# Kernel tuning notes

Measured on AMD Instinct MI355X. Metric: run time of the kernel, lower is better.

## Reference

```python
import jax, jax.numpy as jnp
import numpy as np

N_NODES = 50000
N_EDGES = 800000
K_HOPS = 4
F_IN, F_HID, A_DIM = 6, 128, 3


def gcn_norm(edge_index, edge_weight, num_nodes):
    # TAGConv(normalize=True) uses gcn_norm WITHOUT added self-loops:
    # norm = D^{-1/2}[src] * w * D^{-1/2}[dst], deg computed at target (col).
    row, col = edge_index[0], edge_index[1]
    deg = jax.ops.segment_sum(edge_weight, col, num_segments=num_nodes)
    deg_inv_sqrt = jnp.where(deg > 0, jax.lax.rsqrt(deg), 0.0)
    return deg_inv_sqrt[row] * edge_weight * deg_inv_sqrt[col]


def tag_conv(x, edge_index, norm_w, W, b):
    # out = sum_{k=0..K} (A_hat^k x) @ W[k] + b ; W: [K+1, in, out]
    row, col = edge_index[0], edge_index[1]
    out = x @ W[0]
    xk = x
    for k in range(1, W.shape[0]):
        # one sparse propagation hop: gather at src, scale, scatter-add at dst
        xk = jax.ops.segment_sum(norm_w[:, None] * xk[row], col, num_segments=x.shape[0])
        out = out + xk @ W[k]
    return out + b


def setup_inputs() -> dict:
    key = jax.random.key(0)
    ks = jax.random.split(key, 5)
    x = jax.random.normal(ks[0], (N_NODES, F_IN), dtype=jnp.float32)
    edge_index = jax.random.randint(ks[1], (2, N_EDGES), 0, N_NODES, dtype=jnp.int32)
    edge_weight = jax.random.uniform(ks[2], (N_EDGES,), dtype=jnp.float32)
    s1 = float(1.0 / np.sqrt(F_IN))
    s2 = float(1.0 / np.sqrt(F_HID))
    W1 = jax.random.uniform(ks[3], (K_HOPS + 1, F_IN, F_HID), minval=-s1, maxval=s1, dtype=jnp.float32)
    b1 = jnp.zeros((F_HID,), jnp.float32)
    W2 = jax.random.uniform(ks[4], (K_HOPS + 1, F_HID, 2 * A_DIM), minval=-s2, maxval=s2, dtype=jnp.float32)
    b2 = jnp.zeros((2 * A_DIM,), jnp.float32)
    return {"x": x, "edge_index": edge_index, "edge_weight": edge_weight,
            "W1": W1, "b1": b1, "W2": W2, "b2": b2}


def reference(x, edge_index, edge_weight, W1, b1, W2, b2):
    norm_w = gcn_norm(edge_index, edge_weight, x.shape[0])
    h = jax.nn.relu(tag_conv(x, edge_index, norm_w, W1, b1))
    out = tag_conv(h, edge_index, norm_w, W2, b2)
    mu = jnp.tanh(out[..., :A_DIM])
    logvar = jnp.tanh(out[..., A_DIM:])
    sigma = jnp.exp(2.0 * logvar)
    return mu, sigma
```

## Files before the change

### kernel.cpp

```cpp
#include <hip/hip_runtime.h>

#define NN 50000
#define NE 800000
#define KH 4
#define FIN 6
#define FH 128
#define FO 6
#define ADIM 3
#define NN6 (NN * 6)
#define NN8 (NN * 8)
#define NBKT 196
#define EPB 2048
#define NPB 391
#define CAP 5120
#define ROWMASK 0xFFFFFu
#define GFUSE 2048
#define NEPAD (NE + NBKT * 256)

typedef unsigned int u32;

struct __align__(8) Edge { u32 r; float w; };

__global__ void bucket_hist(const int* __restrict__ col, u32* __restrict__ ghist) {
    __shared__ u32 h[NBKT];
    for (int t = threadIdx.x; t < NBKT; t += 256) h[t] = 0;
    __syncthreads();
    int base = blockIdx.x * EPB;
#pragma unroll
    for (int i = 0; i < EPB / 256; ++i) {
        int e = base + i * 256 + threadIdx.x;
        if (e < NE) atomicAdd(&h[((u32)col[e]) >> 8], 1u);
    }
    __syncthreads();
    for (int t = threadIdx.x; t < NBKT; t += 256)
        if (h[t]) atomicAdd(&ghist[t], h[t]);
}

__global__ void bucket_scan(const u32* __restrict__ ghist, u32* __restrict__ bbase,
                            u32* __restrict__ bcur) {
    __shared__ u32 sh[256];
    int t = threadIdx.x;
    u32 v = (t < NBKT) ? ghist[t] : 0;
    sh[t] = v;
    __syncthreads();
    for (int off = 1; off < 256; off <<= 1) {
        u32 u = (t >= off) ? sh[t - off] : 0;
        __syncthreads();
        sh[t] += u;
        __syncthreads();
    }
    if (t < NBKT) { bbase[t] = sh[t] - v; bcur[t] = sh[t] - v; }
    if (t == NBKT - 1) bbase[NBKT] = sh[t];
}

__global__ __launch_bounds__(256) void partition_kernel(
        const int* __restrict__ row, const int* __restrict__ col,
        const float* __restrict__ w, u32* __restrict__ bcur,
        Edge* __restrict__ etmp) {
    __shared__ u32 hcnt[NBKT];
    __shared__ u32 hloc[NBKT];
    __shared__ u32 hglb[NBKT];
    __shared__ u32 smeta[EPB];
    __shared__ float swt[EPB];
    __shared__ u32 sgid[EPB];
    __shared__ u32 sc[256];
    for (int t = threadIdx.x; t < NBKT; t += 256) hcnt[t] = 0;
    __syncthreads();
    int base = blockIdx.x * EPB;
    u32 m_[8]; float w_[8]; u32 b_[8]; u32 rk_[8]; int v_[8];
#pragma unroll
    for (int i = 0; i < 8; ++i) {
        int e = base + i * 256 + threadIdx.x;
        v_[i] = e < NE;
        if (v_[i]) {
            u32 c = (u32)col[e];
            u32 r = (u32)row[e];
            b_[i] = c >> 8;
            m_[i] = ((c & 255u) << 20) | r;
            w_[i] = w[e];
            rk_[i] = atomicAdd(&hcnt[b_[i]], 1u);
        }
    }
    __syncthreads();
    {
        int t = threadIdx.x;
        u32 v = (t < NBKT) ? hcnt[t] : 0;
        sc[t] = v;
        __syncthreads();
        for (int off = 1; off < 256; off <<= 1) {
            u32 u = (t >= off) ? sc[t - off] : 0;
            __syncthreads();
            sc[t] += u;
            __syncthreads();
        }
        if (t < NBKT) hloc[t] = sc[t] - v;
    }
    __syncthreads();
    for (int t = threadIdx.x; t < NBKT; t += 256)
        if (hcnt[t]) hglb[t] = atomicAdd(&bcur[t], hcnt[t]);
    __syncthreads();
#pragma unroll
    for (int i = 0; i < 8; ++i) if (v_[i]) {
        u32 slot = hloc[b_[i]] + rk_[i];
        smeta[slot] = m_[i];
        swt[slot] = w_[i];
        sgid[slot] = hglb[b_[i]] + rk_[i];
    }
    __syncthreads();
    int tot = NE - base; if (tot > EPB) tot = EPB;
    for (int s = threadIdx.x; s < tot; s += 256) {
        Edge ed; ed.r = smeta[s]; ed.w = swt[s];
        etmp[sgid[s]] = ed;
    }
}

__global__ __launch_bounds__(256) void bucket_csr(
        const u32* __restrict__ bbase, const Edge* __restrict__ etmp,
        Edge* __restrict__ edges, int* __restrict__ offs, int* __restrict__ eoff,
        float* __restrict__ dinv) {
    int b = blockIdx.x;
    int t = threadIdx.x;
    u32 s = bbase[b], e = bbase[b + 1];
    int cnt = (int)(e - s);
    u32 rb = s + (u32)b * 256u;
    int node0 = b << 8;
    int nloc = NN - node0; if (nloc > 256) nloc = 256;
    __shared__ u32 ncnt[256];
    __shared__ float nsum[256];
    __shared__ u32 ncur[256];
    __shared__ u32 sc[256];
    __shared__ Edge stage[CAP];
    ncnt[t] = 0; nsum[t] = 0.f;
    __syncthreads();
    for (int i = t; i < cnt; i += 256) {
        Edge ed = etmp[s + i];
        u32 cl = ed.r >> 20;
        atomicAdd(&ncnt[cl], 1u);
        atomicAdd(&nsum[cl], ed.w);
    }
    __syncthreads();
    u32 v = ncnt[t];
    u32 pv = (v + 1u) & ~1u;
    sc[t] = pv;
    __syncthreads();
    for (int off = 1; off < 256; off <<= 1) {
        u32 u = (t >= off) ? sc[t - off] : 0;
        __syncthreads();
        sc[t] += u;
        __syncthreads();
    }
    u32 excl = sc[t] - pv;
    u32 ptot = sc[255];
    ncur[t] = excl;
    if (t < nloc) {
        offs[node0 + t] = (int)(rb + excl);
        eoff[node0 + t] = (int)(rb + excl + pv);
        float d = nsum[t];
        dinv[node0 + t] = d > 0.f ? rsqrtf(d) : 0.f;
    }
    __syncthreads();
    for (int i = t; i < cnt; i += 256) {
        Edge ed = etmp[s + i];
        u32 cl = ed.r >> 20;
        u32 slot = atomicAdd(&ncur[cl], 1u);
        Edge ce; ce.r = ed.r & ROWMASK; ce.w = ed.w;
        if (slot < CAP) stage[slot] = ce;
        else edges[rb + slot] = ce;
    }
    if (t < nloc && (v & 1u)) {
        u32 slot = excl + v;
        Edge ce; ce.r = 0u; ce.w = 0.f;
        if (slot < CAP) stage[slot] = ce;
        else edges[rb + slot] = ce;
    }
    __syncthreads();
    int lim = (int)(ptot < CAP ? ptot : CAP);
    for (int i = t; i < lim; i += 256) edges[rb + i] = stage[i];
}

__global__ void pad_x(const float* __restrict__ x, float* __restrict__ xpad) {
    int t = blockIdx.x * blockDim.x + threadIdx.x;
    if (t >= NN8) return;
    int n = t >> 3, c = t & 7;
    xpad[t] = (c < 6) ? x[n * 6 + c] : 0.f;
}

__device__ __forceinline__ void gather6(const float* __restrict__ base, u32 r,
                                        int xst, int xof, float w,
                                        float& a0, float& a1, float& a2,
                                        float& a3, float& a4, float& a5) {
    const float* xr = base + (size_t)r * xst + xof;
    float4 u = *(const float4*)xr;
    float2 v = *(const float2*)(xr + 4);
    a0 += w * u.x; a1 += w * u.y; a2 += w * u.z;
    a3 += w * u.w; a4 += w * v.x; a5 += w * v.y;
}

__global__ void hop8(const int* __restrict__ offs, const int* __restrict__ eoff,
                     const Edge* __restrict__ edges,
                     const float* __restrict__ xprev, int xst, int xof,
                     const float* __restrict__ yadd,
                     float* __restrict__ xnext) {
    int t = blockIdx.x * blockDim.x + threadIdx.x;
    int n = t >> 3, j = t & 7;
    if (n >= NN) return;
    int s = offs[n], e = eoff[n];
    float a0 = 0.f, a1 = 0.f, a2 = 0.f, a3 = 0.f, a4 = 0.f, a5 = 0.f;
    for (int i = s + 2 * j; i < e; i += 16) {
        int4 ep = *(const int4*)&edges[i];
        gather6(xprev, (u32)ep.x, xst, xof, __int_as_float(ep.y), a0, a1, a2, a3, a4, a5);
        gather6(xprev, (u32)ep.z, xst, xof, __int_as_float(ep.w), a0, a1, a2, a3, a4, a5);
    }
#pragma unroll
    for (int d = 1; d < 8; d <<= 1) {
        a0 += __shfl_xor(a0, d); a1 += __shfl_xor(a1, d); a2 += __shfl_xor(a2, d);
        a3 += __shfl_xor(a3, d); a4 += __shfl_xor(a4, d); a5 += __shfl_xor(a5, d);
    }
    if (j < 6) {
        float v = j == 0 ? a0 : j == 1 ? a1 : j == 2 ? a2 : j == 3 ? a3 : j == 4 ? a4 : a5;
        if (yadd) v += yadd[(size_t)n * 32 + j];
        xnext[n * 8 + j] = v;
    }
}

__global__ void hop8_norm(const int* __restrict__ offs, const int* __restrict__ eoff,
                          Edge* __restrict__ edges,
                          const float* __restrict__ dinv, const float* __restrict__ xpad,
                          float* __restrict__ xnext) {
    int t = blockIdx.x * blockDim.x + threadIdx.x;
    int n = t >> 3, j = t & 7;
    if (n >= NN) return;
    int s = offs[n], e = eoff[n];
    float dn = dinv[n];
    float a0 = 0.f, a1 = 0.f, a2 = 0.f, a3 = 0.f, a4 = 0.f, a5 = 0.f;
    for (int i = s + 2 * j; i < e; i += 16) {
        int4 ep = *(const int4*)&edges[i];
        u32 r0 = (u32)ep.x, r1 = (u32)ep.z;
        float wn0 = __int_as_float(ep.y) * dn * dinv[r0];
        float wn1 = __int_as_float(ep.w) * dn * dinv[r1];
        ep.y = __float_as_int(wn0); ep.w = __float_as_int(wn1);
        *(int4*)&edges[i] = ep;
        gather6(xpad, r0, 8, 0, wn0, a0, a1, a2, a3, a4, a5);
        gather6(xpad, r1, 8, 0, wn1, a0, a1, a2, a3, a4, a5);
    }
#pragma unroll
    for (int d = 1; d < 8; d <<= 1) {
        a0 += __shfl_xor(a0, d); a1 += __shfl_xor(a1, d); a2 += __shfl_xor(a2, d);
        a3 += __shfl_xor(a3, d); a4 += __shfl_xor(a4, d); a5 += __shfl_xor(a5, d);
    }
    if (j < 6) {
        float v = j == 0 ? a0 : j == 1 ? a1 : j == 2 ? a2 : j == 3 ? a3 : j == 4 ? a4 : a5;
        xnext[n * 8 + j] = v;
    }
}

__global__ void hop8_final(const int* __restrict__ offs, const int* __restrict__ eoff,
                           const Edge* __restrict__ edges,
                           const float* __restrict__ xprev, const float* __restrict__ y0,
                           float* __restrict__ out) {
    int t = blockIdx.x * blockDim.x + threadIdx.x;
    int n = t >> 3, j = t & 7;
    if (n >= NN) return;
    int s = offs[n], e = eoff[n];
    float a0 = 0.f, a1 = 0.f, a2 = 0.f, a3 = 0.f, a4 = 0.f, a5 = 0.f;
    for (int i = s + 2 * j; i < e; i += 16) {
        int4 ep = *(const int4*)&edges[i];
        gather6(xprev, (u32)ep.x, 8, 0, __int_as_float(ep.y), a0, a1, a2, a3, a4, a5);
        gather6(xprev, (u32)ep.z, 8, 0, __int_as_float(ep.w), a0, a1, a2, a3, a4, a5);
    }
#pragma unroll
    for (int d = 1; d < 8; d <<= 1) {
        a0 += __shfl_xor(a0, d); a1 += __shfl_xor(a1, d); a2 += __shfl_xor(a2, d);
        a3 += __shfl_xor(a3, d); a4 += __shfl_xor(a4, d); a5 += __shfl_xor(a5, d);
    }
    if (j < 6) {
        float v = j == 0 ? a0 : j == 1 ? a1 : j == 2 ? a2 : j == 3 ? a3 : j == 4 ? a4 : a5;
        v += y0[(size_t)n * 32 + j];
        float tv = tanhf(v);
        if (j < ADIM) out[n * ADIM + j] = tv;
        else          out[NN * ADIM + n * ADIM + (j - ADIM)] = expf(2.f * tv);
    }
}

__global__ __launch_bounds__(256) void fused_dense_kernel(
        const float* __restrict__ x, const float* __restrict__ xs,
        const float* __restrict__ W1, const float* __restrict__ b1,
        const float* __restrict__ W2, const float* __restrict__ b2,
        float* __restrict__ ys) {
    __shared__ float sin_[2][32];
    __shared__ float sh[2][128];
    int t = threadIdx.x;
    int f = t & 127, half = t >> 7;
    float w1r[30];
#pragma unroll
    for (int i = 0; i < 30; ++i) w1r[i] = W1[i * FH + f];
    float b1r = b1[f];
    bool bact = t < 240;
    int bn = t / 120;
    int rem = t % 120;
    int ka = rem >> 2;
    int q  = rem & 3;
    int k2 = ka / 6, a2 = ka - k2 * 6;
    float w2r[32];
#pragma unroll
    for (int i = 0; i < 32; ++i)
        w2r[i] = bact ? W2[((size_t)k2 * FH + q * 32 + i) * FO + a2] : 0.f;
    float badd = (bact && k2 == 0 && q == 0) ? b2[a2] : 0.f;

    for (int n0 = blockIdx.x * 2; n0 < NN; n0 += GFUSE * 2) {
        if (t < 60) {
            int nn = t / 30, c = t - nn * 30;
            int n = n0 + nn;
            float v;
            if (c < 6) v = x[n * 6 + c];
            else       v = xs[(size_t)((c - 6) / 6) * NN8 + n * 8 + (c - 6) % 6];
            sin_[nn][c] = v;
        }
        __syncthreads();
        {
            float s = b1r;
#pragma unroll
            for (int i = 0; i < 30; ++i) s += sin_[half][i] * w1r[i];
            sh[half][f] = s > 0.f ? s : 0.f;
        }
        __syncthreads();
        if (bact) {
            float s = badd;
            const float* hr = &sh[bn][q * 32];
#pragma unroll
            for (int i = 0; i < 32; ++i) s += hr[i] * w2r[i];
            s += __shfl_xor(s, 1);
            s += __shfl_xor(s, 2);
            if (q == 0) ys[(size_t)(n0 + bn) * 32 + ka] = s;
        }
    }
}

extern "C" void kernel_launch(void* const* d_in, const int* in_sizes, int n_in,
                              void* d_out, int out_size, void* d_ws, size_t ws_size,
                              hipStream_t stream) {
    const float* x  = (const float*)d_in[0];
    const int*   ei = (const int*)d_in[1];
    const float* ew = (const float*)d_in[2];
    const float* W1 = (const float*)d_in[3];
    const float* b1 = (const float*)d_in[4];
    const float* W2 = (const float*)d_in[5];
    const float* b2 = (const float*)d_in[6];
    float* out = (float*)d_out;

    const int* row = ei;
    const int* col = ei + NE;

    Edge*  etmp  = (Edge*)d_ws;
    Edge*  edges = etmp + NE;
    float* xpad  = (float*)(edges + NEPAD);
    float* xs    = xpad + NN8;
    float* ys    = xs + (size_t)KH * NN8;
    float* za    = ys + (size_t)NN * 32;
    float* zb    = za + NN8;
    u32*   ghist = (u32*)(zb + NN8);
    u32*   bbase = ghist + NBKT;
    u32*   bcur  = bbase + NBKT + 1;
    int*   offs  = (int*)(bcur + NBKT);
    int*   eoff  = offs + NN;
    float* dinv  = (float*)(eoff + NN);

    const int B = 256;
    const int gHop = (NN * 8 + B - 1) / B;
    const int gPad = (NN8 + B - 1) / B;

    hipMemsetAsync(ghist, 0, NBKT * sizeof(u32), stream);
    bucket_hist<<<NPB, B, 0, stream>>>(col, ghist);
    bucket_scan<<<1, B, 0, stream>>>(ghist, bbase, bcur);
    partition_kernel<<<NPB, B, 0, stream>>>(row, col, ew, bcur, etmp);
    bucket_csr<<<NBKT, B, 0, stream>>>(bbase, etmp, edges, offs, eoff, dinv);
    pad_x<<<gPad, B, 0, stream>>>(x, xpad);

    hop8_norm<<<gHop, B, 0, stream>>>(offs, eoff, edges, dinv, xpad, xs);
    for (int k = 2; k <= KH; ++k)
        hop8<<<gHop, B, 0, stream>>>(offs, eoff, edges,
                                     xs + (size_t)(k - 2) * NN8, 8, 0, nullptr,
                                     xs + (size_t)(k - 1) * NN8);

    fused_dense_kernel<<<GFUSE, B, 0, stream>>>(x, xs, W1, b1, W2, b2, ys);

    hop8<<<gHop, B, 0, stream>>>(offs, eoff, edges, ys, 32, 24, ys + 18, za);
    hop8<<<gHop, B, 0, stream>>>(offs, eoff, edges, za, 8, 0, ys + 12, zb);
    hop8<<<gHop, B, 0, stream>>>(offs, eoff, edges, zb, 8, 0, ys + 6, za);
    hop8_final<<<gHop, B, 0, stream>>>(offs, eoff, edges, za, ys, out);
}
```

Before: 166.5 us.

## Pack edges and node features into fp16 and use 4 lanes per node

Edges are packed into a single 32-bit word holding a 16-bit row index and an fp16 weight. Node feature vectors in the propagation hops are stored as 8 halfs (16 bytes) instead of 8 floats. Hop kernels now use 4 lanes per node, each handling 4 edges per int4 load, and the CSR padding is raised to multiples of 4. The aim is to halve gather and edge-stream bandwidth in the memory-bound hops, at the cost of fp16 rounding error accumulating over 8 hops.

```diff
diff --git a/kernel.cpp b/kernel.cpp
--- a/kernel.cpp
+++ b/kernel.cpp
@@ -12,14 +12,26 @@
 #define NBKT 196
 #define EPB 2048
 #define NPB 391
-#define CAP 5120
+#define CAP 6144
 #define ROWMASK 0xFFFFFu
 #define GFUSE 2048
-#define NEPAD (NE + NBKT * 256)
+#define NEPAD (NE + NBKT * 1024)
 
 typedef unsigned int u32;
+typedef _Float16 f16;
+typedef f16 f16x8 __attribute__((ext_vector_type(8)));
 
 struct __align__(8) Edge { u32 r; float w; };
+
+__device__ __forceinline__ float h2f_bits(u32 hb) {
+    union { unsigned short us; f16 h; } c; c.us = (unsigned short)hb; return (float)c.h;
+}
+__device__ __forceinline__ u32 f2h_bits(float f) {
+    union { unsigned short us; f16 h; } c; c.h = (f16)f; return (u32)c.us;
+}
+__device__ __forceinline__ u32 pack2(float a, float b) {
+    return f2h_bits(a) | (f2h_bits(b) << 16);
+}
 
 __global__ void bucket_hist(const int* __restrict__ col, u32* __restrict__ ghist) {
     __shared__ u32 h[NBKT];
@@ -116,20 +128,20 @@
 
 __global__ __launch_bounds__(256) void bucket_csr(
         const u32* __restrict__ bbase, const Edge* __restrict__ etmp,
-        Edge* __restrict__ edges, int* __restrict__ offs, int* __restrict__ eoff,
+        u32* __restrict__ edges, int* __restrict__ offs, int* __restrict__ eoff,
         float* __restrict__ dinv) {
     int b = blockIdx.x;
     int t = threadIdx.x;
     u32 s = bbase[b], e = bbase[b + 1];
     int cnt = (int)(e - s);
-    u32 rb = s + (u32)b * 256u;
+    u32 rb = s + (u32)b * 1024u;
     int node0 = b << 8;
     int nloc = NN - node0; if (nloc > 256) nloc = 256;
     __shared__ u32 ncnt[256];
     __shared__ float nsum[256];
     __shared__ u32 ncur[256];
     __shared__ u32 sc[256];
-    __shared__ Edge stage[CAP];
+    __shared__ u32 stage[CAP];
     ncnt[t] = 0; nsum[t] = 0.f;
     __syncthreads();
     for (int i = t; i < cnt; i += 256) {
@@ -140,7 +152,7 @@
     }
     __syncthreads();
     u32 v = ncnt[t];
-    u32 pv = (v + 1u) & ~1u;
+    u32 pv = (v + 3u) & ~3u;
     sc[t] = pv;
     __syncthreads();
     for (int off = 1; off < 256; off <<= 1) {
@@ -163,130 +175,139 @@
         Edge ed = etmp[s + i];
         u32 cl = ed.r >> 20;
         u32 slot = atomicAdd(&ncur[cl], 1u);
-        Edge ce; ce.r = ed.r & ROWMASK; ce.w = ed.w;
-        if (slot < CAP) stage[slot] = ce;
-        else edges[rb + slot] = ce;
-    }
-    if (t < nloc && (v & 1u)) {
-        u32 slot = excl + v;
-        Edge ce; ce.r = 0u; ce.w = 0.f;
-        if (slot < CAP) stage[slot] = ce;
-        else edges[rb + slot] = ce;
+        u32 pw = (ed.r & ROWMASK) | (f2h_bits(ed.w) << 16);
+        if (slot < CAP) stage[slot] = pw;
+        else edges[rb + slot] = pw;
+    }
+    if (t < nloc) {
+        for (u32 slot = excl + v; slot < excl + pv; ++slot) {
+            if (slot < CAP) stage[slot] = 0u;
+            else edges[rb + slot] = 0u;
+        }
     }
     __syncthreads();
     int lim = (int)(ptot < CAP ? ptot : CAP);
     for (int i = t; i < lim; i += 256) edges[rb + i] = stage[i];
 }
 
-__global__ void pad_x(const float* __restrict__ x, float* __restrict__ xpad) {
+__global__ void pad_x(const float* __restrict__ x, f16* __restrict__ xpad) {
     int t = blockIdx.x * blockDim.x + threadIdx.x;
     if (t >= NN8) return;
     int n = t >> 3, c = t & 7;
-    xpad[t] = (c < 6) ? x[n * 6 + c] : 0.f;
-}
-
-__device__ __forceinline__ void gather6(const float* __restrict__ base, u32 r,
-                                        int xst, int xof, float w,
-                                        float& a0, float& a1, float& a2,
-                                        float& a3, float& a4, float& a5) {
-    const float* xr = base + (size_t)r * xst + xof;
-    float4 u = *(const float4*)xr;
-    float2 v = *(const float2*)(xr + 4);
-    a0 += w * u.x; a1 += w * u.y; a2 += w * u.z;
-    a3 += w * u.w; a4 += w * v.x; a5 += w * v.y;
-}
-
-__global__ void hop8(const int* __restrict__ offs, const int* __restrict__ eoff,
-                     const Edge* __restrict__ edges,
-                     const float* __restrict__ xprev, int xst, int xof,
-                     const float* __restrict__ yadd,
-                     float* __restrict__ xnext) {
-    int t = blockIdx.x * blockDim.x + threadIdx.x;
-    int n = t >> 3, j = t & 7;
-    if (n >= NN) return;
-    int s = offs[n], e = eoff[n];
+    xpad[t] = (c < 6) ? (f16)x[n * 6 + c] : (f16)0.f;
+}
+
+__device__ __forceinline__ void gath(const f16* __restrict__ xp, u32 r, float w,
+                                     float& a0, float& a1, float& a2,
+                                     float& a3, float& a4, float& a5) {
+    f16x8 v = *(const f16x8*)(xp + (size_t)r * 8);
+    a0 += w * (float)v[0]; a1 += w * (float)v[1]; a2 += w * (float)v[2];
+    a3 += w * (float)v[3]; a4 += w * (float)v[4]; a5 += w * (float)v[5];
+}
+
+#define HOP_HEAD \
+    int t = blockIdx.x * blockDim.x + threadIdx.x; \
+    int n = t >> 2, j = t & 3; \
+    if (n >= NN) return; \
+    int s = offs[n], e = eoff[n]; \
     float a0 = 0.f, a1 = 0.f, a2 = 0.f, a3 = 0.f, a4 = 0.f, a5 = 0.f;
-    for (int i = s + 2 * j; i < e; i += 16) {
-        int4 ep = *(const int4*)&edges[i];
-        gather6(xprev, (u32)ep.x, xst, xof, __int_as_float(ep.y), a0, a1, a2, a3, a4, a5);
-        gather6(xprev, (u32)ep.z, xst, xof, __int_as_float(ep.w), a0, a1, a2, a3, a4, a5);
-    }
-#pragma unroll
-    for (int d = 1; d < 8; d <<= 1) {
-        a0 += __shfl_xor(a0, d); a1 += __shfl_xor(a1, d); a2 += __shfl_xor(a2, d);
-        a3 += __shfl_xor(a3, d); a4 += __shfl_xor(a4, d); a5 += __shfl_xor(a5, d);
-    }
-    if (j < 6) {
-        float v = j == 0 ? a0 : j == 1 ? a1 : j == 2 ? a2 : j == 3 ? a3 : j == 4 ? a4 : a5;
-        if (yadd) v += yadd[(size_t)n * 32 + j];
-        xnext[n * 8 + j] = v;
-    }
-}
-
-__global__ void hop8_norm(const int* __restrict__ offs, const int* __restrict__ eoff,
-                          Edge* __restrict__ edges,
-                          const float* __restrict__ dinv, const float* __restrict__ xpad,
-                          float* __restrict__ xnext) {
-    int t = blockIdx.x * blockDim.x + threadIdx.x;
-    int n = t >> 3, j = t & 7;
-    if (n >= NN) return;
-    int s = offs[n], e = eoff[n];
+
+#define HOP_REDUCE \
+    _Pragma("unroll") \
+    for (int d = 1; d < 4; d <<= 1) { \
+        a0 += __shfl_xor(a0, d); a1 += __shfl_xor(a1, d); a2 += __shfl_xor(a2, d); \
+        a3 += __shfl_xor(a3, d); a4 += __shfl_xor(a4, d); a5 += __shfl_xor(a5, d); \
+    }
+
+__global__ void hop4(const int* __restrict__ offs, const int* __restrict__ eoff,
+                     const u32* __restrict__ edges,
+                     const f16* __restrict__ xprev, const float* __restrict__ yadd,
+                     f16* __restrict__ xnext) {
+    HOP_HEAD
+    for (int i = s + 4 * j; i < e; i += 16) {
+        int4 q = *(const int4*)(edges + i);
+        { u32 wd = (u32)q.x; gath(xprev, wd & 0xFFFFu, h2f_bits(wd >> 16), a0, a1, a2, a3, a4, a5); }
+        { u32 wd = (u32)q.y; gath(xprev, wd & 0xFFFFu, h2f_bits(wd >> 16), a0, a1, a2, a3, a4, a5); }
+        { u32 wd = (u32)q.z; gath(xprev, wd & 0xFFFFu, h2f_bits(wd >> 16), a0, a1, a2, a3, a4, a5); }
+        { u32 wd = (u32)q.w; gath(xprev, wd & 0xFFFFu, h2f_bits(wd >> 16), a0, a1, a2, a3, a4, a5); }
+    }
+    HOP_REDUCE
+    float v0 = j == 0 ? a0 : j == 1 ? a2 : j == 2 ? a4 : 0.f;
+    float v1 = j == 0 ? a1 : j == 1 ? a3 : j == 2 ? a5 : 0.f;
+    if (yadd && j < 3) {
+        v0 += yadd[(size_t)n * 32 + 2 * j];
+        v1 += yadd[(size_t)n * 32 + 2 * j + 1];
+    }
+    ((u32*)xnext)[(size_t)n * 4 + j] = pack2(v0, v1);
+}
+
+__global__ void hop4_norm(const int* __restrict__ offs, const int* __restrict__ eoff,
+                          u32* __restrict__ edges,
+                          const float* __restrict__ dinv, const f16* __restrict__ xpad,
+                          f16* __restrict__ xnext) {
+    HOP_HEAD
     float dn = dinv[n];
-    float a0 = 0.f, a1 = 0.f, a2 = 0.f, a3 = 0.f, a4 = 0.f, a5 = 0.f;
-    for (int i = s + 2 * j; i < e; i += 16) {
-        int4 ep = *(const int4*)&edges[i];
-        u32 r0 = (u32)ep.x, r1 = (u32)ep.z;
-        float wn0 = __int_as_float(ep.y) * dn * dinv[r0];
-        float wn1 = __int_as_float(ep.w) * dn * dinv[r1];
-        ep.y = __float_as_int(wn0); ep.w = __float_as_int(wn1);
-        *(int4*)&edges[i] = ep;
-        gather6(xpad, r0, 8, 0, wn0, a0, a1, a2, a3, a4, a5);
-        gather6(xpad, r1, 8, 0, wn1, a0, a1, a2, a3, a4, a5);
-    }
-#pragma unroll
-    for (int d = 1; d < 8; d <<= 1) {
-        a0 += __shfl_xor(a0, d); a1 += __shfl_xor(a1, d); a2 += __shfl_xor(a2, d);
-        a3 += __shfl_xor(a3, d); a4 += __shfl_xor(a4, d); a5 += __shfl_xor(a5, d);
-    }
-    if (j < 6) {
-        float v = j == 0 ? a0 : j == 1 ? a1 : j == 2 ? a2 : j == 3 ? a3 : j == 4 ? a4 : a5;
-        xnext[n * 8 + j] = v;
-    }
-}
-
-__global__ void hop8_final(const int* __restrict__ offs, const int* __restrict__ eoff,
-                           const Edge* __restrict__ edges,
-                           const float* __restrict__ xprev, const float* __restrict__ y0,
+    for (int i = s + 4 * j; i < e; i += 16) {
+        int4 q = *(const int4*)(edges + i);
+        int4 nq;
+        {
+            u32 wd = (u32)q.x; u32 r = wd & 0xFFFFu;
+            float wn = h2f_bits(wd >> 16) * dn * dinv[r];
+            nq.x = (int)(r | (f2h_bits(wn) << 16));
+            gath(xpad, r, wn, a0, a1, a2, a3, a4, a5);
+        }
+        {
+            u32 wd = (u32)q.y; u32 r = wd & 0xFFFFu;
+            float wn = h2f_bits(wd >> 16) * dn * dinv[r];
+            nq.y = (int)(r | (f2h_bits(wn) << 16));
+            gath(xpad, r, wn, a0, a1, a2, a3, a4, a5);
+        }
+        {
+            u32 wd = (u32)q.z; u32 r = wd & 0xFFFFu;
+            float wn = h2f_bits(wd >> 16) * dn * dinv[r];
+            nq.z = (int)(r | (f2h_bits(wn) << 16));
+            gath(xpad, r, wn, a0, a1, a2, a3, a4, a5);
+        }
+        {
+            u32 wd = (u32)q.w; u32 r = wd & 0xFFFFu;
+            float wn = h2f_bits(wd >> 16) * dn * dinv[r];
+            nq.w = (int)(r | (f2h_bits(wn) << 16));
+            gath(xpad, r, wn, a0, a1, a2, a3, a4, a5);
+        }
+        *(int4*)(edges + i) = nq;
+    }
+    HOP_REDUCE
+    float v0 = j == 0 ? a0 : j == 1 ? a2 : j == 2 ? a4 : 0.f;
+    float v1 = j == 0 ? a1 : j == 1 ? a3 : j == 2 ? a5 : 0.f;
+    ((u32*)xnext)[(size_t)n * 4 + j] = pack2(v0, v1);
+}
+
+__global__ void hop4_final(const int* __restrict__ offs, const int* __restrict__ eoff,
+                           const u32* __restrict__ edges,
+                           const f16* __restrict__ xprev, const float* __restrict__ y0,
                            float* __restrict__ out) {
-    int t = blockIdx.x * blockDim.x + threadIdx.x;
-    int n = t >> 3, j = t & 7;
-    if (n >= NN) return;
-    int s = offs[n], e = eoff[n];
-    float a0 = 0.f, a1 = 0.f, a2 = 0.f, a3 = 0.f, a4 = 0.f, a5 = 0.f;
-    for (int i = s + 2 * j; i < e; i += 16) {
-        int4 ep = *(const int4*)&edges[i];
-        gather6(xprev, (u32)ep.x, 8, 0, __int_as_float(ep.y), a0, a1, a2, a3, a4, a5);
-        gather6(xprev, (u32)ep.z, 8, 0, __int_as_float(ep.w), a0, a1, a2, a3, a4, a5);
-    }
-#pragma unroll
-    for (int d = 1; d < 8; d <<= 1) {
-        a0 += __shfl_xor(a0, d); a1 += __shfl_xor(a1, d); a2 += __shfl_xor(a2, d);
-        a3 += __shfl_xor(a3, d); a4 += __shfl_xor(a4, d); a5 += __shfl_xor(a5, d);
-    }
-    if (j < 6) {
-        float v = j == 0 ? a0 : j == 1 ? a1 : j == 2 ? a2 : j == 3 ? a3 : j == 4 ? a4 : a5;
-        v += y0[(size_t)n * 32 + j];
-        float tv = tanhf(v);
-        if (j < ADIM) out[n * ADIM + j] = tv;
-        else          out[NN * ADIM + n * ADIM + (j - ADIM)] = expf(2.f * tv);
+    HOP_HEAD
+    for (int i = s + 4 * j; i < e; i += 16) {
+        int4 q = *(const int4*)(edges + i);
+        { u32 wd = (u32)q.x; gath(xprev, wd & 0xFFFFu, h2f_bits(wd >> 16), a0, a1, a2, a3, a4, a5); }
+        { u32 wd = (u32)q.y; gath(xprev, wd & 0xFFFFu, h2f_bits(wd >> 16), a0, a1, a2, a3, a4, a5); }
+        { u32 wd = (u32)q.z; gath(xprev, wd & 0xFFFFu, h2f_bits(wd >> 16), a0, a1, a2, a3, a4, a5); }
+        { u32 wd = (u32)q.w; gath(xprev, wd & 0xFFFFu, h2f_bits(wd >> 16), a0, a1, a2, a3, a4, a5); }
+    }
+    HOP_REDUCE
+    if (j < 3) {
+        float mv = (j == 0 ? a0 : j == 1 ? a1 : a2) + y0[(size_t)n * 32 + j];
+        float sv = (j == 0 ? a3 : j == 1 ? a4 : a5) + y0[(size_t)n * 32 + 3 + j];
+        out[n * ADIM + j] = tanhf(mv);
+        out[NN * ADIM + n * ADIM + j] = expf(2.f * tanhf(sv));
     }
 }
 
 __global__ __launch_bounds__(256) void fused_dense_kernel(
-        const float* __restrict__ x, const float* __restrict__ xs,
+        const float* __restrict__ x, const f16* __restrict__ xs,
         const float* __restrict__ W1, const float* __restrict__ b1,
         const float* __restrict__ W2, const float* __restrict__ b2,
-        float* __restrict__ ys) {
+        float* __restrict__ ys, f16* __restrict__ y4h) {
     __shared__ float sin_[2][32];
     __shared__ float sh[2][128];
     int t = threadIdx.x;
@@ -313,7 +334,7 @@
             int n = n0 + nn;
             float v;
             if (c < 6) v = x[n * 6 + c];
-            else       v = xs[(size_t)((c - 6) / 6) * NN8 + n * 8 + (c - 6) % 6];
+            else       v = (float)xs[(size_t)((c - 6) / 6) * NN8 + n * 8 + (c - 6) % 6];
             sin_[nn][c] = v;
         }
         __syncthreads();
@@ -331,7 +352,10 @@
             for (int i = 0; i < 32; ++i) s += hr[i] * w2r[i];
             s += __shfl_xor(s, 1);
             s += __shfl_xor(s, 2);
-            if (q == 0) ys[(size_t)(n0 + bn) * 32 + ka] = s;
+            if (q == 0) {
+                if (ka < 24) ys[(size_t)(n0 + bn) * 32 + ka] = s;
+                else         y4h[(size_t)(n0 + bn) * 8 + (ka - 24)] = (f16)s;
+            }
         }
     }
 }
@@ -351,14 +375,15 @@
     const int* row = ei;
     const int* col = ei + NE;
 
-    Edge*  etmp  = (Edge*)d_ws;
-    Edge*  edges = etmp + NE;
-    float* xpad  = (float*)(edges + NEPAD);
-    float* xs    = xpad + NN8;
-    float* ys    = xs + (size_t)KH * NN8;
-    float* za    = ys + (size_t)NN * 32;
-    float* zb    = za + NN8;
-    u32*   ghist = (u32*)(zb + NN8);
+    f16*   xpad  = (f16*)d_ws;
+    f16*   xs    = xpad + NN8;
+    f16*   y4h   = xs + (size_t)KH * NN8;
+    f16*   za    = y4h + NN8;
+    f16*   zb    = za + NN8;
+    float* ys    = (float*)(zb + NN8);
+    Edge*  etmp  = (Edge*)(ys + (size_t)NN * 32);
+    u32*   edges = (u32*)(etmp + NE);
+    u32*   ghist = edges + NEPAD;
     u32*   bbase = ghist + NBKT;
     u32*   bcur  = bbase + NBKT + 1;
     int*   offs  = (int*)(bcur + NBKT);
@@ -366,7 +391,7 @@
     float* dinv  = (float*)(eoff + NN);
 
     const int B = 256;
-    const int gHop = (NN * 8 + B - 1) / B;
+    const int gHop = (NN * 4 + B - 1) / B;
     const int gPad = (NN8 + B - 1) / B;
 
     hipMemsetAsync(ghist, 0, NBKT * sizeof(u32), stream);
@@ -376,16 +401,16 @@
     bucket_csr<<<NBKT, B, 0, stream>>>(bbase, etmp, edges, offs, eoff, dinv);
     pad_x<<<gPad, B, 0, stream>>>(x, xpad);
 
-    hop8_norm<<<gHop, B, 0, stream>>>(offs, eoff, edges, dinv, xpad, xs);
+    hop4_norm<<<gHop, B, 0, stream>>>(offs, eoff, edges, dinv, xpad, xs);
     for (int k = 2; k <= KH; ++k)
-        hop8<<<gHop, B, 0, stream>>>(offs, eoff, edges,
-                                     xs + (size_t)(k - 2) * NN8, 8, 0, nullptr,
+        hop4<<<gHop, B, 0, stream>>>(offs, eoff, edges,
+                                     xs + (size_t)(k - 2) * NN8, nullptr,
                                      xs + (size_t)(k - 1) * NN8);
 
-    fused_dense_kernel<<<GFUSE, B, 0, stream>>>(x, xs, W1, b1, W2, b2, ys);
-
-    hop8<<<gHop, B, 0, stream>>>(offs, eoff, edges, ys, 32, 24, ys + 18, za);
-    hop8<<<gHop, B, 0, stream>>>(offs, eoff, edges, za, 8, 0, ys + 12, zb);
-    hop8<<<gHop, B, 0, stream>>>(offs, eoff, edges, zb, 8, 0, ys + 6, za);
-    hop8_final<<<gHop, B, 0, stream>>>(offs, eoff, edges, za, ys, out);
-}
+    fused_dense_kernel<<<GFUSE, B, 0, stream>>>(x, xs, W1, b1, W2, b2, ys, y4h);
+
+    hop4<<<gHop, B, 0, stream>>>(offs, eoff, edges, y4h, ys + 18, za);
+    hop4<<<gHop, B, 0, stream>>>(offs, eoff, edges, za, ys + 12, zb);
+    hop4<<<gHop, B, 0, stream>>>(offs, eoff, edges, zb, ys + 6, za);
+    hop4_final<<<gHop, B, 0, stream>>>(offs, eoff, edges, za, ys, out);
+}
```

Result: faster. 153.4 us (-7.9%).
